# Kernel optimization log

Measured on AMD Instinct MI355X. Metric: run time of the kernel, lower is better.

## Reference

```python
import jax, jax.numpy as jnp
import numpy as np

DN = ('NCHW', 'OIHW', 'NCHW')


def _conv(x, w, b, pad):
    y = jax.lax.conv_general_dilated(x, w, window_strides=(1, 1),
                                     padding=[(pad, pad), (pad, pad)],
                                     dimension_numbers=DN)
    return y + b[None, :, None, None]


def _maxpool2(x):
    return jax.lax.reduce_window(x, -jnp.inf, jax.lax.max,
                                 (1, 1, 2, 2), (1, 1, 2, 2), 'VALID')


def setup_inputs() -> dict:
    key = jax.random.key(0)
    ks = jax.random.split(key, 17)
    s = 0.05
    inp = {
        'x':  jax.random.normal(ks[0], (256, 3, 32, 32), jnp.float32),
        # conv weights (OIHW) and biases, matching AlexNet_flags.features
        'w1': jax.random.normal(ks[1], (64, 3, 3, 3), jnp.float32) * s,
        'b1': jax.random.normal(ks[2], (64,), jnp.float32) * s,
        'w2': jax.random.normal(ks[3], (192, 64, 5, 5), jnp.float32) * s,
        'b2': jax.random.normal(ks[4], (192,), jnp.float32) * s,
        'w3': jax.random.normal(ks[5], (384, 192, 3, 3), jnp.float32) * s,
        'b3': jax.random.normal(ks[6], (384,), jnp.float32) * s,
        'w4': jax.random.normal(ks[7], (256, 384, 3, 3), jnp.float32) * s,
        'b4': jax.random.normal(ks[8], (256,), jnp.float32) * s,
        'w5': jax.random.normal(ks[9], (256, 256, 3, 3), jnp.float32) * s,
        'b5': jax.random.normal(ks[10], (256,), jnp.float32) * s,
        # classifier linears (weight stored [out, in] as in torch)
        'fw1': jax.random.normal(ks[11], (4096, 256 * 4 * 4), jnp.float32) * s,
        'fb1': jax.random.normal(ks[12], (4096,), jnp.float32) * s,
        'fw2': jax.random.normal(ks[13], (4096, 4096), jnp.float32) * s,
        'fb2': jax.random.normal(ks[14], (4096,), jnp.float32) * s,
        'fw3': jax.random.normal(ks[15], (1000, 4096), jnp.float32) * s,
        'fb3': jax.random.normal(ks[16], (1000,), jnp.float32) * s,
    }
    return inp


def reference(x, w1, b1, w2, b2, w3, b3, w4, b4, w5, b5,
              fw1, fb1, fw2, fb2, fw3, fb3):
    relu = jax.nn.relu
    h = _maxpool2(relu(_conv(x, w1, b1, pad=1)))   # [B,64,16,16]
    h = _maxpool2(relu(_conv(h, w2, b2, pad=2)))   # [B,192,8,8]
    h = relu(_conv(h, w3, b3, pad=1))              # [B,384,8,8]
    h = relu(_conv(h, w4, b4, pad=1))              # [B,256,8,8]
    h = _maxpool2(relu(_conv(h, w5, b5, pad=1)))   # [B,256,4,4]
    h = h.reshape(h.shape[0], 256 * 4 * 4)
    # Dropout layers act as identity at inference (eval mode).
    h = relu(h @ fw1.T + fb1)
    h = relu(h @ fw2.T + fb2)
    return h @ fw3.T + fb3                          # [B,1000]
```

## Files before the change

### kernel.cpp

```cpp
#include <hip/hip_runtime.h>
#include <hip/hip_bf16.h>

#define DIV_UP(a,b) (((a)+(b)-1)/(b))

typedef __attribute__((ext_vector_type(8))) short bfrag;
typedef __attribute__((ext_vector_type(4))) float accf;

__device__ __forceinline__ unsigned short f2bf(float f) {
    __hip_bfloat16 h = __float2bfloat16(f);
    return *reinterpret_cast<unsigned short*>(&h);
}

__global__ __launch_bounds__(256) void conv1_mfma(
    const float* __restrict__ in, const float* __restrict__ w,
    const float* __restrict__ bias, unsigned short* __restrict__ out, int n0)
{
    constexpr int RAWS = 3 * 6 * 34;
    constexpr int INS  = 128 * 32;
    constexpr int WSZ  = 64 * 32;
    constexpr int CS   = 128 * 66;
    constexpr int SMEM = (CS * 4 > (RAWS + 4 + INS + WSZ) * 2)
                       ? CS * 4 : (RAWS + 4 + INS + WSZ) * 2;
    __shared__ __align__(16) char smem[SMEM];
    short* raw_s = (short*)smem;
    short* in_s  = raw_s + RAWS + 4;
    short* w_s   = in_s + INS;
    float* c_s   = (float*)smem;

    const int tid  = threadIdx.x;
    const int lane = tid & 63, wv = tid >> 6;
    const int quad = lane >> 4, lr = lane & 15;
    const int rb   = blockIdx.x;
    const int nl   = blockIdx.y;
    const int n    = n0 + nl;
    const int row0 = rb * 4;

    for (int idx = tid; idx < RAWS; idx += 256) {
        int c = idx / 204, rem = idx - c * 204;
        int ry = rem / 34, rx = rem - ry * 34;
        int iy = row0 - 1 + ry, ix = rx - 1;
        float v = 0.f;
        if (iy >= 0 && iy < 32 && ix >= 0 && ix < 32)
            v = in[((n * 3 + c) * 32 + iy) * 32 + ix];
        raw_s[idx] = (short)f2bf(v);
    }
    {
        const int soc = tid >> 2, cbq = tid & 3;
        const int wsw = ((cbq ^ ((soc >> 1) & 3)) << 3);
        __align__(16) unsigned short buf[8];
#pragma unroll
        for (int j = 0; j < 8; ++j) {
            int k = cbq * 8 + j;
            buf[j] = (k < 27) ? f2bf(w[soc * 27 + k]) : (unsigned short)0;
        }
        *(uint4*)&w_s[soc * 32 + wsw] = *(uint4*)buf;
    }
    __syncthreads();
    {
        const int k = tid & 31, pg = tid >> 5;
        const int shi = k >> 3, slo = k & 7;
        const bool valid = (k < 27);
        int cbase = 0;
        if (valid) {
            int c = k / 9, rr = k - c * 9;
            int ky = rr / 3, kx = rr - ky * 3;
            cbase = c * 204 + ky * 34 + kx;
        }
        const int prow = pg >> 1, pcol0 = (pg & 1) * 16;
        const int rbase = cbase + prow * 34 + pcol0;
#pragma unroll
        for (int i = 0; i < 16; ++i) {
            const int pos = prow * 32 + pcol0 + i;
            short v = valid ? raw_s[rbase + i] : (short)0;
            in_s[pos * 32 + ((shi ^ ((pos >> 1) & 3)) << 3) + slo] = v;
        }
    }
    __syncthreads();
    const int bswz = (quad ^ ((lr >> 1) & 3)) << 3;
    const bfrag b = *(const bfrag*)(w_s + (wv * 16 + lr) * 32 + bswz);
    accf acc[8];
#pragma unroll
    for (int mt = 0; mt < 8; ++mt) {
        const int pos = mt * 16 + lr;
        const bfrag a = *(const bfrag*)(in_s + pos * 32 + ((quad ^ ((pos >> 1) & 3)) << 3));
        acc[mt] = __builtin_amdgcn_mfma_f32_16x16x32_bf16(
            a, b, (accf){0.f, 0.f, 0.f, 0.f}, 0, 0, 0);
    }
    __syncthreads();
#pragma unroll
    for (int mt = 0; mt < 8; ++mt)
#pragma unroll
        for (int r = 0; r < 4; ++r)
            c_s[(mt * 16 + quad * 4 + r) * 66 + wv * 16 + lr] = acc[mt][r];
    __syncthreads();
    {
        const int oc = tid >> 2;
        const float bv = bias[oc];
        const int o0 = (tid & 3) * 8;
        __align__(16) unsigned short buf[8];
#pragma unroll
        for (int i = 0; i < 8; ++i) {
            int op = o0 + i, oy = op >> 4, ox = op & 15;
            int p = (oy * 2) * 32 + ox * 2;
            float v = fmaxf(fmaxf(c_s[p * 66 + oc],        c_s[(p + 1) * 66 + oc]),
                            fmaxf(c_s[(p + 32) * 66 + oc], c_s[(p + 33) * 66 + oc]));
            buf[i] = f2bf(fmaxf(v + bv, 0.f));
        }
        unsigned short* dst = out + ((size_t)(nl * 64 + oc)) * 256 + (row0 >> 1) * 16 + o0;
        *(uint4*)dst = *(uint4*)buf;
    }
}

__global__ __launch_bounds__(256) void wt_transform(
    const float* __restrict__ w, unsigned short* __restrict__ wt,
    int COUT, int CIN, int KK, int total)
{
    int idx = blockIdx.x * 256 + threadIdx.x;
    if (idx >= total) return;
    const int ci = idx & 31;
    int t = idx >> 5;
    const int oc = t % COUT; t /= COUT;
    const int NC = CIN >> 5;
    const int cc = t % NC;
    const int k  = t / NC;
    wt[idx] = f2bf(w[((size_t)oc * CIN + cc * 32 + ci) * KK + k]);
}

template<int CIN, int KS, int HIN, int MROWS, int MODE, int KG, int COUT>
__global__ __launch_bounds__(256) void conv_mfma(
    const unsigned short* __restrict__ in, const unsigned short* __restrict__ wt,
    const float* __restrict__ bias, unsigned short* __restrict__ out)
{
    constexpr int PAD  = KS / 2;
    constexpr int KK   = KS * KS;
    constexpr int PIX  = HIN * HIN;
    constexpr int M    = MROWS * HIN;
    constexpr int MT   = M / 16;
    constexpr int ROWB = HIN / MROWS;
    constexpr int NC   = CIN / 32;
    constexpr int INS  = PIX * 32 + 32;
    constexpr int WSZ  = KG * 64 * 32;
    constexpr int CS   = M * 66;
    constexpr int SMEM = ((INS + WSZ) * 2 > CS * 4) ? (INS + WSZ) * 2 : CS * 4;

    __shared__ __align__(16) char smem[SMEM];
    short* in_s = (short*)smem;
    short* w_s  = in_s + INS;
    float* c_s  = (float*)smem;

    const int tid  = threadIdx.x;
    const int lane = tid & 63, wv = tid >> 6;
    const int quad = lane >> 4, lr = lane & 15;
    const int ocb  = blockIdx.x / ROWB, rb = blockIdx.x % ROWB;
    const int oc0  = ocb * 64;
    const int nl   = blockIdx.y;
    const int row0 = rb * MROWS;

    if (tid < 32) in_s[PIX * 32 + tid] = 0;

    accf acc[MT];
#pragma unroll
    for (int i = 0; i < MT; ++i) acc[i] = (accf){0.f, 0.f, 0.f, 0.f};

    const int bswz = (quad ^ ((lr >> 1) & 3)) << 3;

    int pym[MT], pxm[MT];
#pragma unroll
    for (int mt = 0; mt < MT; ++mt) {
        const int m = mt * 16 + lr;
        pym[mt] = row0 + m / HIN;
        pxm[mt] = m % HIN;
    }
    int apos[KG][MT];
    if constexpr (KG == KK) {
#pragma unroll
        for (int g = 0; g < KK; ++g) {
            const int dy = g / KS - PAD, dx = g % KS - PAD;
#pragma unroll
            for (int mt = 0; mt < MT; ++mt) {
                const int iy = pym[mt] + dy, ix = pxm[mt] + dx;
                const bool ok = ((unsigned)iy < (unsigned)HIN) &
                                ((unsigned)ix < (unsigned)HIN);
                const int pos = ok ? (iy * HIN + ix) : PIX;
                apos[g][mt] = pos * 64 + ((quad ^ ((pos >> 1) & 3)) << 4);
            }
        }
    }

    const int sci = tid & 31, slot = tid >> 5;
    const int shi = sci >> 3, slo = sci & 7;
    const int soc = tid >> 2, cbq = tid & 3;
    const int wsw = ((cbq ^ ((soc >> 1) & 3)) << 3);

    for (int c0 = 0; c0 < CIN; c0 += 32) {
#pragma unroll
        for (int kg = 0; kg < KK; kg += KG) {
            __syncthreads();
            if (kg == 0) {
                const unsigned short* src = in + ((size_t)(nl * CIN + c0 + sci)) * PIX;
                for (int iy = slot; iy < HIN; iy += 8) {
#pragma unroll
                    for (int xc = 0; xc < HIN; xc += 8) {
                        uint4 v = *(const uint4*)(src + iy * HIN + xc);
                        const int p0 = iy * HIN + xc;
                        unsigned short e[8];
                        e[0] = (unsigned short)(v.x & 0xFFFF); e[1] = (unsigned short)(v.x >> 16);
                        e[2] = (unsigned short)(v.y & 0xFFFF); e[3] = (unsigned short)(v.y >> 16);
                        e[4] = (unsigned short)(v.z & 0xFFFF); e[5] = (unsigned short)(v.z >> 16);
                        e[6] = (unsigned short)(v.w & 0xFFFF); e[7] = (unsigned short)(v.w >> 16);
#pragma unroll
                        for (int k = 0; k < 8; ++k) {
                            const int p = p0 + k;
                            in_s[p * 32 + ((shi ^ ((p >> 1) & 3)) << 3) + slo] = (short)e[k];
                        }
                    }
                }
            }
            {
#pragma unroll
                for (int g = 0; g < KG; ++g) {
                    const unsigned short* wp = wt +
                        (((size_t)(kg + g) * NC + (c0 >> 5)) * COUT + oc0 + soc) * 32 + cbq * 8;
                    *(uint4*)&w_s[(g * 64 + soc) * 32 + wsw] = *(const uint4*)wp;
                }
            }
            __syncthreads();
#pragma unroll
            for (int g = 0; g < KG; ++g) {
                const bfrag b = *(const bfrag*)(w_s + (g * 64 + wv * 16 + lr) * 32 + bswz);
                if constexpr (KG == KK) {
#pragma unroll
                    for (int mt = 0; mt < MT; ++mt) {
                        const bfrag a = *(const bfrag*)((const char*)in_s + apos[g][mt]);
                        acc[mt] = __builtin_amdgcn_mfma_f32_16x16x32_bf16(a, b, acc[mt], 0, 0, 0);
                    }
                } else {
                    const int kidx = kg + g;
                    const int dy = kidx / KS - PAD, dx = kidx % KS - PAD;
#pragma unroll
                    for (int mt = 0; mt < MT; ++mt) {
                        const int iy = pym[mt] + dy, ix = pxm[mt] + dx;
                        const bool ok = ((unsigned)iy < (unsigned)HIN) &
                                        ((unsigned)ix < (unsigned)HIN);
                        const int pos = ok ? (iy * HIN + ix) : PIX;
                        const bfrag a = *(const bfrag*)(in_s + pos * 32 +
                                          ((quad ^ ((pos >> 1) & 3)) << 3));
                        acc[mt] = __builtin_amdgcn_mfma_f32_16x16x32_bf16(a, b, acc[mt], 0, 0, 0);
                    }
                }
            }
        }
    }

    __syncthreads();
#pragma unroll
    for (int mt = 0; mt < MT; ++mt)
#pragma unroll
        for (int r = 0; r < 4; ++r)
            c_s[(mt * 16 + quad * 4 + r) * 66 + wv * 16 + lr] = acc[mt][r];
    __syncthreads();

    const int oc = tid >> 2;
    const float bv = bias[oc0 + oc];
    if (MODE == 0) {
        const int p0 = (tid & 3) * (M / 4);
        __align__(16) unsigned short buf[16];
#pragma unroll
        for (int i = 0; i < 16; ++i)
            buf[i] = f2bf(fmaxf(c_s[(p0 + i) * 66 + oc] + bv, 0.f));
        unsigned short* dst = out + ((size_t)(nl * COUT + oc0 + oc)) * PIX + row0 * HIN + p0;
        *(uint4*)(dst)     = *(uint4*)(buf);
        *(uint4*)(dst + 8) = *(uint4*)(buf + 8);
    } else if (MODE == 1) {
        constexpr int OW = HIN / 2;
        constexpr int OM = (MROWS / 2) * OW;
        const int o0 = (tid & 3) * (OM / 4);
        __align__(16) unsigned short buf[OM / 4];
#pragma unroll
        for (int i = 0; i < OM / 4; ++i) {
            int op = o0 + i, oy = op / OW, ox = op % OW;
            int p = (oy * 2) * HIN + ox * 2;
            float v = fmaxf(fmaxf(c_s[p * 66 + oc],        c_s[(p + 1) * 66 + oc]),
                            fmaxf(c_s[(p + HIN) * 66 + oc], c_s[(p + HIN + 1) * 66 + oc]));
            buf[i] = f2bf(fmaxf(v + bv, 0.f));
        }
        unsigned short* dst = out + ((size_t)(nl * COUT + oc0 + oc)) * (PIX / 4)
                            + (row0 / 2) * OW + o0;
        *(uint4*)dst = *(uint4*)buf;
    } else {
        const int o0 = (tid & 3) * 4;
        __align__(16) unsigned short buf[4];
#pragma unroll
        for (int i = 0; i < 4; ++i) {
            int op = o0 + i, oy = op >> 2, ox = op & 3;
            int p = (oy * 2) * 8 + ox * 2;
            float v = fmaxf(fmaxf(c_s[p * 66 + oc],       c_s[(p + 8) * 66 + oc]),
                            fmaxf(c_s[(p + 1) * 66 + oc], c_s[(p + 9) * 66 + oc]));
            buf[i] = f2bf(fmaxf(v + bv, 0.f));
        }
        *(uint2*)(out + (size_t)nl * 4096 + (oc0 + oc) * 16 + o0) = *(uint2*)buf;
    }
}

template<bool RELU, bool F32OUT>
__global__ __launch_bounds__(1024) void fc_mfma4(
    const unsigned short* __restrict__ X, const float* __restrict__ W,
    const float* __restrict__ Bs, void* __restrict__ Yv, int N, int K)
{
    __shared__ __align__(16) char smem[65536];
    short* stag = (short*)smem;
    float* red  = (float*)smem;

    const int tid  = threadIdx.x;
    const int lane = tid & 63;
    const int w16  = tid >> 6;
    const int grp  = w16 >> 2;
    const int wg   = w16 & 3;
    const int quad = lane >> 4, lr = lane & 15;
    const int m0 = blockIdx.y * 64, n0 = blockIdx.x * 64;
    const int gtid = tid & 255;
    const int mm = gtid >> 2, ko = (gtid & 3) * 8;
    const int KQ = K >> 2;

    short* Xs = stag + grp * 4096;
    short* Ws = Xs + 2048;

    accf acc[4];
#pragma unroll
    for (int i = 0; i < 4; ++i) acc[i] = (accf){0.f, 0.f, 0.f, 0.f};

    int nr = n0 + mm; if (nr > N - 1) nr = N - 1;
    const unsigned short* xp = X + (size_t)(m0 + mm) * K + (size_t)grp * KQ + ko;
    const float*          wp = W + (size_t)nr * K + (size_t)grp * KQ + ko;

    const int wsw = (((gtid & 3) ^ ((mm >> 1) & 3)) << 3);
    const int rsw = ((quad ^ ((lr >> 1) & 3)) << 3);

    uint4  xv = *(const uint4*)(xp);
    float4 wa = *(const float4*)(wp);
    float4 wb = *(const float4*)(wp + 4);

    for (int k0 = 0; k0 < KQ; k0 += 32) {
        __syncthreads();
        *(uint4*)&Xs[mm * 32 + wsw] = xv;
        __align__(16) unsigned short wb16[8] = {
            f2bf(wa.x), f2bf(wa.y), f2bf(wa.z), f2bf(wa.w),
            f2bf(wb.x), f2bf(wb.y), f2bf(wb.z), f2bf(wb.w) };
        *(uint4*)&Ws[mm * 32 + wsw] = *(uint4*)wb16;
        __syncthreads();
        if (k0 + 32 < KQ) {
            xv = *(const uint4*)(xp + k0 + 32);
            wa = *(const float4*)(wp + k0 + 32);
            wb = *(const float4*)(wp + k0 + 36);
        }
        const bfrag b = *(const bfrag*)(Ws + (wg * 16 + lr) * 32 + rsw);
#pragma unroll
        for (int mt = 0; mt < 4; ++mt) {
            const bfrag a = *(const bfrag*)(Xs + (mt * 16 + lr) * 32 + rsw);
            acc[mt] = __builtin_amdgcn_mfma_f32_16x16x32_bf16(a, b, acc[mt], 0, 0, 0);
        }
    }

    __syncthreads();
#pragma unroll
    for (int mt = 0; mt < 4; ++mt)
#pragma unroll
        for (int r = 0; r < 4; ++r)
            red[grp * 4096 + (mt * 16 + quad * 4 + r) * 64 + wg * 16 + lr] = acc[mt][r];
    __syncthreads();

    {
        const int m  = tid >> 4;
        const int nq = (tid & 15) * 4;
        float4 v0 = *(const float4*)&red[            m * 64 + nq];
        float4 v1 = *(const float4*)&red[ 4096 +     m * 64 + nq];
        float4 v2 = *(const float4*)&red[ 8192 +     m * 64 + nq];
        float4 v3 = *(const float4*)&red[12288 +     m * 64 + nq];
        float s[4] = { v0.x + v1.x + v2.x + v3.x,
                       v0.y + v1.y + v2.y + v3.y,
                       v0.z + v1.z + v2.z + v3.z,
                       v0.w + v1.w + v2.w + v3.w };
#pragma unroll
        for (int i = 0; i < 4; ++i) {
            const int n = n0 + nq + i;
            if (n < N) {
                float v = s[i] + Bs[n];
                if (RELU) v = fmaxf(v, 0.f);
                if (F32OUT) ((float*)Yv)[(size_t)(m0 + m) * N + n] = v;
                else ((unsigned short*)Yv)[(size_t)(m0 + m) * N + n] = f2bf(v);
            }
        }
    }
}

__global__ void zero_out(float* __restrict__ out, int total)
{
    int i = blockIdx.x * 256 + threadIdx.x;
    if (i < total) out[i] = 0.f;
}

extern "C" void kernel_launch(void* const* d_in, const int* in_sizes, int n_in,
                              void* d_out, int out_size, void* d_ws, size_t ws_size,
                              hipStream_t stream)
{
    (void)in_sizes; (void)n_in;
    const float* x   = (const float*)d_in[0];
    const float* w1  = (const float*)d_in[1];
    const float* b1  = (const float*)d_in[2];
    const float* w2  = (const float*)d_in[3];
    const float* b2  = (const float*)d_in[4];
    const float* w3  = (const float*)d_in[5];
    const float* b3  = (const float*)d_in[6];
    const float* w4  = (const float*)d_in[7];
    const float* b4  = (const float*)d_in[8];
    const float* w5  = (const float*)d_in[9];
    const float* b5  = (const float*)d_in[10];
    const float* fw1 = (const float*)d_in[11];
    const float* fb1 = (const float*)d_in[12];
    const float* fw2 = (const float*)d_in[13];
    const float* fb2 = (const float*)d_in[14];
    const float* fw3 = (const float*)d_in[15];
    const float* fb3 = (const float*)d_in[16];
    float* out = (float*)d_out;

    const size_t WTB = 4890624u;
    int maxCH;
    if      (ws_size >= 27959296u) maxCH = 256;
    else if (ws_size >= 17473536u) maxCH = 128;
    else if (ws_size >= 14852096u) maxCH = 96;
    else if (ws_size >= 12230656u) maxCH = 64;
    else {
        zero_out<<<DIV_UP(out_size, 256), 256, 0, stream>>>(out, out_size);
        return;
    }
    unsigned short* wt2 = (unsigned short*)d_ws;
    unsigned short* wt3 = wt2 + 307200;
    unsigned short* wt4 = wt3 + 663552;
    unsigned short* wt5 = wt4 + 884736;
    const size_t CAb = ((size_t)maxCH * 49152u > 2097152u) ? (size_t)maxCH * 49152u : 2097152u;
    const size_t CBb = ((size_t)maxCH * 32768u > 2097152u) ? (size_t)maxCH * 32768u : 2097152u;
    unsigned short* CA = (unsigned short*)((char*)d_ws + WTB);
    unsigned short* CB = (unsigned short*)((char*)d_ws + WTB + CAb);
    unsigned short* T5 = (unsigned short*)((char*)d_ws + WTB + CAb + CBb);

    wt_transform<<<DIV_UP(307200, 256), 256, 0, stream>>>(w2, wt2, 192, 64, 25, 307200);
    wt_transform<<<DIV_UP(663552, 256), 256, 0, stream>>>(w3, wt3, 384, 192, 9, 663552);
    wt_transform<<<DIV_UP(884736, 256), 256, 0, stream>>>(w4, wt4, 256, 384, 9, 884736);
    wt_transform<<<DIV_UP(589824, 256), 256, 0, stream>>>(w5, wt5, 256, 256, 9, 589824);

    for (int n0 = 0; n0 < 256; ) {
        const int CH = (256 - n0 < maxCH) ? (256 - n0) : maxCH;
        conv1_mfma<<<dim3(8, CH), 256, 0, stream>>>(x, w1, b1, CA, n0);
        conv_mfma<64, 5, 16, 8, 1, 5, 192><<<dim3(6, CH), 256, 0, stream>>>(CA, wt2, b2, CB);
        conv_mfma<192, 3, 8, 8, 0, 9, 384><<<dim3(6, CH), 256, 0, stream>>>(CB, wt3, b3, CA);
        conv_mfma<384, 3, 8, 8, 0, 9, 256><<<dim3(4, CH), 256, 0, stream>>>(CA, wt4, b4, CB);
        conv_mfma<256, 3, 8, 8, 2, 9, 256><<<dim3(4, CH), 256, 0, stream>>>(
            CB, wt5, b5, T5 + (size_t)n0 * 4096);
        n0 += CH;
    }

    fc_mfma4<true, false><<<dim3(64, 4), 1024, 0, stream>>>(T5, fw1, fb1, CA, 4096, 4096);
    fc_mfma4<true, false><<<dim3(64, 4), 1024, 0, stream>>>(CA, fw2, fb2, CB, 4096, 4096);
    fc_mfma4<false, true><<<dim3(16, 4), 1024, 0, stream>>>(CB, fw3, fb3, out, 1000, 4096);
}
```

Baseline: 527.6 us.

## Switch conv layers to 32x32x16 MFMA with register-streamed weights and 2-image tiles

Replaces the 16x16x32 MFMA convolution kernel with one built on 32x32x16 bf16 MFMA. Weights are pre-arranged into a fragment-ready layout and loaded straight from global memory into registers, with the next tap prefetched, so the shared-memory weight staging and its barriers go away. The 8x8 layers now process two images per block so each block covers a 128-row M tile. The trade-offs are fewer blocks for those layers, more global weight traffic per wave, and possible exposed load latency. It also assumes CH is even.

Result: faster. 504.4 us (-4.4%).

```diff
diff --git a/kernel.cpp b/kernel.cpp
--- a/kernel.cpp
+++ b/kernel.cpp
@@ -5,6 +5,7 @@
 
 typedef __attribute__((ext_vector_type(8))) short bfrag;
 typedef __attribute__((ext_vector_type(4))) float accf;
+typedef __attribute__((ext_vector_type(16))) float accf16;
 
 __device__ __forceinline__ unsigned short f2bf(float f) {
     __hip_bfloat16 h = __float2bfloat16(f);
@@ -117,188 +118,196 @@
 {
     int idx = blockIdx.x * 256 + threadIdx.x;
     if (idx >= total) return;
-    const int ci = idx & 31;
-    int t = idx >> 5;
-    const int oc = t % COUT; t /= COUT;
-    const int NC = CIN >> 5;
-    const int cc = t % NC;
-    const int k  = t / NC;
-    wt[idx] = f2bf(w[((size_t)oc * CIN + cc * 32 + ci) * KK + k]);
-}
-
-template<int CIN, int KS, int HIN, int MROWS, int MODE, int KG, int COUT>
-__global__ __launch_bounds__(256) void conv_mfma(
+    const int j    = idx & 7;
+    const int lane = (idx >> 3) & 63;
+    const int kh   = (idx >> 9) & 1;
+    int t = idx >> 10;
+    const int NOCG = COUT >> 5;
+    const int ocg  = t % NOCG; t /= NOCG;
+    const int NC   = CIN >> 5;
+    const int cc   = t % NC;
+    const int g    = t / NC;
+    const int oc = ocg * 32 + (lane & 31);
+    const int ci = cc * 32 + kh * 16 + (lane >> 5) * 8 + j;
+    wt[idx] = f2bf(w[((size_t)oc * CIN + ci) * KK + g]);
+}
+
+template<int CIN, int KS, int HIN, int IMGS, int MODE, int COUT>
+__global__ __launch_bounds__(256) void conv_mfma32(
     const unsigned short* __restrict__ in, const unsigned short* __restrict__ wt,
     const float* __restrict__ bias, unsigned short* __restrict__ out)
 {
     constexpr int PAD  = KS / 2;
     constexpr int KK   = KS * KS;
     constexpr int PIX  = HIN * HIN;
-    constexpr int M    = MROWS * HIN;
-    constexpr int MT   = M / 16;
-    constexpr int ROWB = HIN / MROWS;
     constexpr int NC   = CIN / 32;
-    constexpr int INS  = PIX * 32 + 32;
-    constexpr int WSZ  = KG * 64 * 32;
-    constexpr int CS   = M * 66;
-    constexpr int SMEM = ((INS + WSZ) * 2 > CS * 4) ? (INS + WSZ) * 2 : CS * 4;
+    constexpr int NOCG = COUT / 32;
+    constexpr int IPOS = IMGS * PIX;
+    constexpr int ROWB = (IMGS == 1) ? PIX / 128 : 1;
+    constexpr int INS  = IPOS * 32 + 32;
+    constexpr int CS   = 128 * 66;
+    constexpr int SMEM = (INS * 2 > CS * 4) ? INS * 2 : CS * 4;
+    constexpr int GSTR = NC * NOCG * 1024;
 
     __shared__ __align__(16) char smem[SMEM];
     short* in_s = (short*)smem;
-    short* w_s  = in_s + INS;
     float* c_s  = (float*)smem;
 
     const int tid  = threadIdx.x;
     const int lane = tid & 63, wv = tid >> 6;
-    const int quad = lane >> 4, lr = lane & 15;
+    const int hi   = lane >> 5, lr32 = lane & 31;
+    const int wvM  = wv >> 1, wvN = wv & 1;
     const int ocb  = blockIdx.x / ROWB, rb = blockIdx.x % ROWB;
     const int oc0  = ocb * 64;
-    const int nl   = blockIdx.y;
-    const int row0 = rb * MROWS;
-
-    if (tid < 32) in_s[PIX * 32 + tid] = 0;
-
-    accf acc[MT];
-#pragma unroll
-    for (int i = 0; i < MT; ++i) acc[i] = (accf){0.f, 0.f, 0.f, 0.f};
-
-    const int bswz = (quad ^ ((lr >> 1) & 3)) << 3;
-
-    int pym[MT], pxm[MT];
-#pragma unroll
-    for (int mt = 0; mt < MT; ++mt) {
-        const int m = mt * 16 + lr;
+    const int nl0  = (IMGS == 2) ? blockIdx.y * 2 : blockIdx.y;
+    const int row0 = rb * (128 / HIN);
+
+    if (tid < 32) in_s[IPOS * 32 + tid] = 0;
+
+    accf16 acc[2];
+#pragma unroll
+    for (int i = 0; i < 2; ++i)
+#pragma unroll
+        for (int r = 0; r < 16; ++r) acc[i][r] = 0.f;
+
+    int pym[2], pxm[2];
+#pragma unroll
+    for (int mt = 0; mt < 2; ++mt) {
+        const int m = wvM * 64 + mt * 32 + lr32;
         pym[mt] = row0 + m / HIN;
         pxm[mt] = m % HIN;
     }
-    int apos[KG][MT];
-    if constexpr (KG == KK) {
+    int apos[KK][2];
+    if constexpr (KS == 3) {
 #pragma unroll
         for (int g = 0; g < KK; ++g) {
-            const int dy = g / KS - PAD, dx = g % KS - PAD;
-#pragma unroll
-            for (int mt = 0; mt < MT; ++mt) {
-                const int iy = pym[mt] + dy, ix = pxm[mt] + dx;
-                const bool ok = ((unsigned)iy < (unsigned)HIN) &
-                                ((unsigned)ix < (unsigned)HIN);
-                const int pos = ok ? (iy * HIN + ix) : PIX;
-                apos[g][mt] = pos * 64 + ((quad ^ ((pos >> 1) & 3)) << 4);
+            const int dy = g / 3 - 1, dx = g % 3 - 1;
+#pragma unroll
+            for (int mt = 0; mt < 2; ++mt) {
+                const int m = wvM * 64 + mt * 32 + lr32;
+                const int img = m >> 6, p = m & 63;
+                const int iy = (p >> 3) + dy, ix = (p & 7) + dx;
+                const bool ok = ((unsigned)iy < 8u) & ((unsigned)ix < 8u);
+                const int pos = ok ? img * 64 + iy * 8 + ix : IPOS;
+                apos[g][mt] = pos * 64 + ((hi ^ ((pos >> 1) & 3)) << 4);
             }
         }
     }
 
     const int sci = tid & 31, slot = tid >> 5;
     const int shi = sci >> 3, slo = sci & 7;
-    const int soc = tid >> 2, cbq = tid & 3;
-    const int wsw = ((cbq ^ ((soc >> 1) & 3)) << 3);
+    const unsigned short* wbase = wt + (size_t)(oc0 / 32 + wvN) * 1024 + lane * 8;
 
     for (int c0 = 0; c0 < CIN; c0 += 32) {
-#pragma unroll
-        for (int kg = 0; kg < KK; kg += KG) {
-            __syncthreads();
-            if (kg == 0) {
-                const unsigned short* src = in + ((size_t)(nl * CIN + c0 + sci)) * PIX;
-                for (int iy = slot; iy < HIN; iy += 8) {
-#pragma unroll
-                    for (int xc = 0; xc < HIN; xc += 8) {
-                        uint4 v = *(const uint4*)(src + iy * HIN + xc);
-                        const int p0 = iy * HIN + xc;
-                        unsigned short e[8];
-                        e[0] = (unsigned short)(v.x & 0xFFFF); e[1] = (unsigned short)(v.x >> 16);
-                        e[2] = (unsigned short)(v.y & 0xFFFF); e[3] = (unsigned short)(v.y >> 16);
-                        e[4] = (unsigned short)(v.z & 0xFFFF); e[5] = (unsigned short)(v.z >> 16);
-                        e[6] = (unsigned short)(v.w & 0xFFFF); e[7] = (unsigned short)(v.w >> 16);
-#pragma unroll
-                        for (int k = 0; k < 8; ++k) {
-                            const int p = p0 + k;
-                            in_s[p * 32 + ((shi ^ ((p >> 1) & 3)) << 3) + slo] = (short)e[k];
-                        }
+        const unsigned short* wb = wbase + (size_t)(c0 >> 5) * (NOCG * 1024);
+        __syncthreads();
+#pragma unroll
+        for (int img = 0; img < IMGS; ++img) {
+            const unsigned short* src = in + ((size_t)((nl0 + img) * CIN + c0 + sci)) * PIX;
+            for (int iy = slot; iy < HIN; iy += 8) {
+#pragma unroll
+                for (int xc = 0; xc < HIN; xc += 8) {
+                    uint4 v = *(const uint4*)(src + iy * HIN + xc);
+                    const int p0 = img * PIX + iy * HIN + xc;
+                    unsigned short e[8];
+                    e[0] = (unsigned short)(v.x & 0xFFFF); e[1] = (unsigned short)(v.x >> 16);
+                    e[2] = (unsigned short)(v.y & 0xFFFF); e[3] = (unsigned short)(v.y >> 16);
+                    e[4] = (unsigned short)(v.z & 0xFFFF); e[5] = (unsigned short)(v.z >> 16);
+                    e[6] = (unsigned short)(v.w & 0xFFFF); e[7] = (unsigned short)(v.w >> 16);
+#pragma unroll
+                    for (int k = 0; k < 8; ++k) {
+                        const int p = p0 + k;
+                        in_s[p * 32 + ((shi ^ ((p >> 1) & 3)) << 3) + slo] = (short)e[k];
                     }
                 }
             }
-            {
-#pragma unroll
-                for (int g = 0; g < KG; ++g) {
-                    const unsigned short* wp = wt +
-                        (((size_t)(kg + g) * NC + (c0 >> 5)) * COUT + oc0 + soc) * 32 + cbq * 8;
-                    *(uint4*)&w_s[(g * 64 + soc) * 32 + wsw] = *(const uint4*)wp;
+        }
+        bfrag bc0 = *(const bfrag*)(wb);
+        bfrag bc1 = *(const bfrag*)(wb + 512);
+        __syncthreads();
+#pragma unroll
+        for (int g = 0; g < KK; ++g) {
+            bfrag bn0 = bc0, bn1 = bc1;
+            if (g + 1 < KK) {
+                bn0 = *(const bfrag*)(wb + (size_t)(g + 1) * GSTR);
+                bn1 = *(const bfrag*)(wb + (size_t)(g + 1) * GSTR + 512);
+            }
+            int ap[2];
+            if constexpr (KS == 3) {
+                ap[0] = apos[g][0]; ap[1] = apos[g][1];
+            } else {
+                const int dy = g / KS - PAD, dx = g % KS - PAD;
+#pragma unroll
+                for (int mt = 0; mt < 2; ++mt) {
+                    const int iy = pym[mt] + dy, ix = pxm[mt] + dx;
+                    const bool ok = ((unsigned)iy < (unsigned)HIN) &
+                                    ((unsigned)ix < (unsigned)HIN);
+                    const int pos = ok ? iy * HIN + ix : IPOS;
+                    ap[mt] = pos * 64 + ((hi ^ ((pos >> 1) & 3)) << 4);
                 }
             }
-            __syncthreads();
-#pragma unroll
-            for (int g = 0; g < KG; ++g) {
-                const bfrag b = *(const bfrag*)(w_s + (g * 64 + wv * 16 + lr) * 32 + bswz);
-                if constexpr (KG == KK) {
-#pragma unroll
-                    for (int mt = 0; mt < MT; ++mt) {
-                        const bfrag a = *(const bfrag*)((const char*)in_s + apos[g][mt]);
-                        acc[mt] = __builtin_amdgcn_mfma_f32_16x16x32_bf16(a, b, acc[mt], 0, 0, 0);
-                    }
-                } else {
-                    const int kidx = kg + g;
-                    const int dy = kidx / KS - PAD, dx = kidx % KS - PAD;
-#pragma unroll
-                    for (int mt = 0; mt < MT; ++mt) {
-                        const int iy = pym[mt] + dy, ix = pxm[mt] + dx;
-                        const bool ok = ((unsigned)iy < (unsigned)HIN) &
-                                        ((unsigned)ix < (unsigned)HIN);
-                        const int pos = ok ? (iy * HIN + ix) : PIX;
-                        const bfrag a = *(const bfrag*)(in_s + pos * 32 +
-                                          ((quad ^ ((pos >> 1) & 3)) << 3));
-                        acc[mt] = __builtin_amdgcn_mfma_f32_16x16x32_bf16(a, b, acc[mt], 0, 0, 0);
-                    }
+#pragma unroll
+            for (int kh = 0; kh < 2; ++kh) {
+                const bfrag bb = kh ? bc1 : bc0;
+#pragma unroll
+                for (int mt = 0; mt < 2; ++mt) {
+                    const bfrag a = *(const bfrag*)((const char*)in_s + (ap[mt] ^ (kh << 5)));
+                    acc[mt] = __builtin_amdgcn_mfma_f32_32x32x16_bf16(a, bb, acc[mt], 0, 0, 0);
                 }
             }
-        }
-    }
-
-    __syncthreads();
-#pragma unroll
-    for (int mt = 0; mt < MT; ++mt)
-#pragma unroll
-        for (int r = 0; r < 4; ++r)
-            c_s[(mt * 16 + quad * 4 + r) * 66 + wv * 16 + lr] = acc[mt][r];
+            bc0 = bn0; bc1 = bn1;
+        }
+    }
+
+    __syncthreads();
+#pragma unroll
+    for (int mt = 0; mt < 2; ++mt)
+#pragma unroll
+        for (int r = 0; r < 16; ++r) {
+            const int row = wvM * 64 + mt * 32 + (r & 3) + 8 * (r >> 2) + 4 * hi;
+            c_s[row * 66 + wvN * 32 + lr32] = acc[mt][r];
+        }
     __syncthreads();
 
     const int oc = tid >> 2;
     const float bv = bias[oc0 + oc];
     if (MODE == 0) {
-        const int p0 = (tid & 3) * (M / 4);
-        __align__(16) unsigned short buf[16];
-#pragma unroll
-        for (int i = 0; i < 16; ++i)
-            buf[i] = f2bf(fmaxf(c_s[(p0 + i) * 66 + oc] + bv, 0.f));
-        unsigned short* dst = out + ((size_t)(nl * COUT + oc0 + oc)) * PIX + row0 * HIN + p0;
-        *(uint4*)(dst)     = *(uint4*)(buf);
-        *(uint4*)(dst + 8) = *(uint4*)(buf + 8);
+        const int q = tid & 3, img = q >> 1, pl0 = (q & 1) * 32;
+        __align__(16) unsigned short buf[32];
+#pragma unroll
+        for (int i = 0; i < 32; ++i)
+            buf[i] = f2bf(fmaxf(c_s[(img * 64 + pl0 + i) * 66 + oc] + bv, 0.f));
+        unsigned short* dst = out + ((size_t)((nl0 + img) * COUT + oc0 + oc)) * 64 + pl0;
+        *(uint4*)(dst)      = *(uint4*)(buf);
+        *(uint4*)(dst + 8)  = *(uint4*)(buf + 8);
+        *(uint4*)(dst + 16) = *(uint4*)(buf + 16);
+        *(uint4*)(dst + 24) = *(uint4*)(buf + 24);
     } else if (MODE == 1) {
-        constexpr int OW = HIN / 2;
-        constexpr int OM = (MROWS / 2) * OW;
-        const int o0 = (tid & 3) * (OM / 4);
-        __align__(16) unsigned short buf[OM / 4];
-#pragma unroll
-        for (int i = 0; i < OM / 4; ++i) {
-            int op = o0 + i, oy = op / OW, ox = op % OW;
-            int p = (oy * 2) * HIN + ox * 2;
+        const int o0 = (tid & 3) * 8;
+        __align__(16) unsigned short buf[8];
+#pragma unroll
+        for (int i = 0; i < 8; ++i) {
+            int op = o0 + i, oy = op >> 3, ox = op & 7;
+            int p = (oy * 2) * 16 + ox * 2;
             float v = fmaxf(fmaxf(c_s[p * 66 + oc],        c_s[(p + 1) * 66 + oc]),
-                            fmaxf(c_s[(p + HIN) * 66 + oc], c_s[(p + HIN + 1) * 66 + oc]));
+                            fmaxf(c_s[(p + 16) * 66 + oc], c_s[(p + 17) * 66 + oc]));
             buf[i] = f2bf(fmaxf(v + bv, 0.f));
         }
-        unsigned short* dst = out + ((size_t)(nl * COUT + oc0 + oc)) * (PIX / 4)
-                            + (row0 / 2) * OW + o0;
+        unsigned short* dst = out + ((size_t)(nl0 * COUT + oc0 + oc)) * 64
+                            + (row0 >> 1) * 8 + o0;
         *(uint4*)dst = *(uint4*)buf;
     } else {
-        const int o0 = (tid & 3) * 4;
-        __align__(16) unsigned short buf[4];
-#pragma unroll
-        for (int i = 0; i < 4; ++i) {
+        const int q = tid & 3, img = q >> 1, o0 = (q & 1) * 8;
+        __align__(16) unsigned short buf[8];
+#pragma unroll
+        for (int i = 0; i < 8; ++i) {
             int op = o0 + i, oy = op >> 2, ox = op & 3;
-            int p = (oy * 2) * 8 + ox * 2;
-            float v = fmaxf(fmaxf(c_s[p * 66 + oc],       c_s[(p + 8) * 66 + oc]),
-                            fmaxf(c_s[(p + 1) * 66 + oc], c_s[(p + 9) * 66 + oc]));
+            int p = img * 64 + (oy * 2) * 8 + ox * 2;
+            float v = fmaxf(fmaxf(c_s[p * 66 + oc],       c_s[(p + 1) * 66 + oc]),
+                            fmaxf(c_s[(p + 8) * 66 + oc], c_s[(p + 9) * 66 + oc]));
             buf[i] = f2bf(fmaxf(v + bv, 0.f));
         }
-        *(uint2*)(out + (size_t)nl * 4096 + (oc0 + oc) * 16 + o0) = *(uint2*)buf;
+        *(uint4*)(out + (size_t)(nl0 + img) * 4096 + (oc0 + oc) * 16 + o0) = *(uint4*)buf;
     }
 }
 
@@ -451,10 +460,10 @@
     for (int n0 = 0; n0 < 256; ) {
         const int CH = (256 - n0 < maxCH) ? (256 - n0) : maxCH;
         conv1_mfma<<<dim3(8, CH), 256, 0, stream>>>(x, w1, b1, CA, n0);
-        conv_mfma<64, 5, 16, 8, 1, 5, 192><<<dim3(6, CH), 256, 0, stream>>>(CA, wt2, b2, CB);
-        conv_mfma<192, 3, 8, 8, 0, 9, 384><<<dim3(6, CH), 256, 0, stream>>>(CB, wt3, b3, CA);
-        conv_mfma<384, 3, 8, 8, 0, 9, 256><<<dim3(4, CH), 256, 0, stream>>>(CA, wt4, b4, CB);
-        conv_mfma<256, 3, 8, 8, 2, 9, 256><<<dim3(4, CH), 256, 0, stream>>>(
+        conv_mfma32<64, 5, 16, 1, 1, 192><<<dim3(6, CH), 256, 0, stream>>>(CA, wt2, b2, CB);
+        conv_mfma32<192, 3, 8, 2, 0, 384><<<dim3(6, CH / 2), 256, 0, stream>>>(CB, wt3, b3, CA);
+        conv_mfma32<384, 3, 8, 2, 0, 256><<<dim3(4, CH / 2), 256, 0, stream>>>(CA, wt4, b4, CB);
+        conv_mfma32<256, 3, 8, 2, 2, 256><<<dim3(4, CH / 2), 256, 0, stream>>>(
             CB, wt5, b5, T5 + (size_t)n0 * 4096);
         n0 += CH;
     }
```
